# Performance work log

Hardware: AMD Instinct MI355X
Metric: run time of the kernel (lower is better)

## Reference

```python
import jax, jax.numpy as jnp
import numpy as np

N, E = 50000, 800000
IN_DIM, OUT_DIM, HEADS, ORDER = 128, 32, 4, 2
HID = OUT_DIM * HEADS  # 128
NEG_SLOPE = 0.2
LN_EPS = 1e-5


def setup_inputs() -> dict:
    key = jax.random.key(0)
    ks = jax.random.split(key, 16)
    inp = {
        'features': jax.random.normal(ks[0], (N, IN_DIM), jnp.float32),
        'src': jax.random.randint(ks[1], (E,), 0, N, jnp.int32),
        'dst': jax.random.randint(ks[2], (E,), 0, N, jnp.int32),
    }
    in_dims = [IN_DIM, HID]
    for i in range(ORDER):
        d_in = in_dims[i]
        s = 1.0 / np.sqrt(d_in)
        inp[f'W{i}'] = jax.random.normal(ks[3 + 5 * i], (d_in, HID), jnp.float32) * s
        inp[f'al{i}'] = jax.random.normal(ks[4 + 5 * i], (HEADS, OUT_DIM), jnp.float32) * 0.1
        inp[f'ar{i}'] = jax.random.normal(ks[5 + 5 * i], (HEADS, OUT_DIM), jnp.float32) * 0.1
        inp[f'b{i}'] = jnp.zeros((HID,), jnp.float32)
        inp[f'g{i}'] = jnp.ones((HID,), jnp.float32)
        inp[f'be{i}'] = jnp.zeros((HID,), jnp.float32)
    return inp


def _gat_layer(x, src, dst, W, al, ar, b):
    # x: [N, d_in] -> h: [N, H, D]
    h = (x @ W).reshape(N, HEADS, OUT_DIM)
    el = jnp.sum(h * al, axis=-1)  # [N, H]
    er = jnp.sum(h * ar, axis=-1)  # [N, H]
    e = jax.nn.leaky_relu(el[src] + er[dst], NEG_SLOPE)  # [E, H]
    # segment softmax over incoming edges of each dst node
    m = jax.ops.segment_max(e, dst, num_segments=N)  # [N, H]
    ex = jnp.exp(e - m[dst])  # [E, H]
    denom = jax.ops.segment_sum(ex, dst, num_segments=N)  # [N, H]
    alpha = ex / jnp.maximum(denom[dst], 1e-9)  # [E, H]
    msg = h[src] * alpha[:, :, None]  # [E, H, D]
    out = jax.ops.segment_sum(msg, dst, num_segments=N)  # [N, H, D]
    return out.reshape(N, HID) + b


def _layernorm(x, g, be):
    mu = jnp.mean(x, axis=-1, keepdims=True)
    var = jnp.mean(jnp.square(x - mu), axis=-1, keepdims=True)
    return (x - mu) * jax.lax.rsqrt(var + LN_EPS) * g + be


def reference(features, src, dst, W0, al0, ar0, b0, g0, be0, W1, al1, ar1, b1, g1, be1):
    feats = features
    params = [(W0, al0, ar0, b0, g0, be0), (W1, al1, ar1, b1, g1, be1)]
    for (W, al, ar, b, g, be) in params:
        feats = _gat_layer(feats, src, dst, W, al, ar, b)
        feats = _layernorm(feats, g, be)
        feats = jax.nn.elu(feats)
    return feats
```

## Files before the change

### kernel.cpp

```cpp
#include <hip/hip_runtime.h>
#include <hip/hip_bf16.h>

#define N_NODES 50000
#define E_EDGES 800000
#define HID 128
#define HEADS 4
#define NEG_SLOPE 0.2f
#define LN_EPS 1e-5f
#define PARAM_FLOATS 17024
#define NBUCK 196
#define BCAP 6144
#define BIN_CH 2048

typedef __attribute__((ext_vector_type(8))) short short8;
typedef __attribute__((ext_vector_type(4))) float float4v;

__device__ __forceinline__ float bf2f(__hip_bfloat16 b) { return __bfloat162float(b); }
__device__ __forceinline__ float u2f(unsigned short u) {
    return __uint_as_float(((unsigned int)u) << 16);
}
__device__ __forceinline__ short bfb(float f) {
    __hip_bfloat16 h = __float2bfloat16(f);
    return *(short*)&h;
}
__device__ __forceinline__ float leaky(float v) { return v > 0.f ? v : v * NEG_SLOPE; }

__device__ __forceinline__ unsigned int f2ord(float f) {
    unsigned int u = __float_as_uint(f);
    return (u & 0x80000000u) ? ~u : (u | 0x80000000u);
}
__device__ __forceinline__ float ord2f(unsigned int u) {
    u = (u & 0x80000000u) ? (u & 0x7FFFFFFFu) : ~u;
    return __uint_as_float(u);
}

__global__ __launch_bounds__(256) void detect_kernel(const unsigned int* __restrict__ w0,
                                                     unsigned int* __restrict__ flag,
                                                     unsigned int* __restrict__ gmax0,
                                                     unsigned int* __restrict__ gmax1) {
    int t = threadIdx.x;
    if (t < 4) {
        gmax0[t] = f2ord(-INFINITY);
        gmax1[t] = f2ord(-INFINITY);
    }
    int cnt = 0;
    for (int i = t; i < 4096; i += 256) {
        unsigned int lo = (w0[i] & 0xFFFFu) << 16;
        float v = fabsf(__uint_as_float(lo));
        if (v >= 1e-6f && v <= 1.0f) cnt++;
    }
    __shared__ int sh[4];
#pragma unroll
    for (int off = 32; off >= 1; off >>= 1) cnt += __shfl_xor(cnt, off);
    if ((t & 63) == 0) sh[t >> 6] = cnt;
    __syncthreads();
    if (t == 0) *flag = ((sh[0] + sh[1] + sh[2] + sh[3]) > 2048) ? 1u : 0u;
}

__device__ __forceinline__ float load_any(const void* p, int i, unsigned int isbf16) {
    return isbf16 ? bf2f(((const __hip_bfloat16*)p)[i]) : ((const float*)p)[i];
}

__global__ __launch_bounds__(256) void cvt_params_kernel(const void* W, const void* al,
                                                         const void* ar, const void* b,
                                                         const void* g, const void* be,
                                                         const unsigned int* __restrict__ flag,
                                                         float* __restrict__ out,
                                                         unsigned short* __restrict__ wt) {
    int i = blockIdx.x * 256 + threadIdx.x;
    if (i >= PARAM_FLOATS) return;
    unsigned int isb = *flag;
    if (i < 16384) {
        unsigned short bits;
        if (isb) bits = ((const unsigned short*)W)[i];
        else     { short s = bfb(((const float*)W)[i]); bits = (unsigned short)s; }
        wt[((i & 127) << 7) | (i >> 7)] = bits;
        return;
    }
    const void* src; int off;
    if (i < 16512)      { src = al; off = i - 16384; }
    else if (i < 16640) { src = ar; off = i - 16512; }
    else if (i < 16768) { src = b;  off = i - 16640; }
    else if (i < 16896) { src = g;  off = i - 16768; }
    else                { src = be; off = i - 16896; }
    out[i] = load_any(src, off, isb);
}

__global__ __launch_bounds__(256) void bin_kernel(const int* __restrict__ src,
                                                  const int* __restrict__ dst,
                                                  int* __restrict__ bcnt,
                                                  unsigned int* __restrict__ ebuf) {
    __shared__ int lh[NBUCK];
    __shared__ int lbase[NBUCK];
    int t = threadIdx.x;
    for (int i = t; i < NBUCK; i += 256) lh[i] = 0;
    __syncthreads();
    int e0 = blockIdx.x * BIN_CH;
    int n = min(BIN_CH, E_EDGES - e0);
    int s8[8], d8[8], rk[8];
#pragma unroll
    for (int j = 0; j < 8; ++j) {
        int k = j * 256 + t;
        if (k < n) {
            s8[j] = src[e0 + k];
            d8[j] = dst[e0 + k];
            rk[j] = atomicAdd(&lh[d8[j] >> 8], 1);
        }
    }
    __syncthreads();
    for (int i = t; i < NBUCK; i += 256) lbase[i] = atomicAdd(&bcnt[i], lh[i]);
    __syncthreads();
#pragma unroll
    for (int j = 0; j < 8; ++j) {
        int k = j * 256 + t;
        if (k < n) {
            int b = d8[j] >> 8;
            int pos = lbase[b] + rk[j];
            if (pos < BCAP)
                ebuf[b * BCAP + pos] = ((unsigned int)s8[j] << 8) | (unsigned int)(d8[j] & 255);
        }
    }
}

__global__ __launch_bounds__(256) void bscan_kernel(const int* __restrict__ bcnt,
                                                    int* __restrict__ bbase) {
    int t = threadIdx.x;
    int lane = t & 63, wid = t >> 6;
    int v = (t < NBUCK) ? min(bcnt[t], BCAP) : 0;
    int x = v;
#pragma unroll
    for (int o = 1; o < 64; o <<= 1) {
        int y = __shfl_up(x, o);
        if (lane >= o) x += y;
    }
    __shared__ int wt[4];
    if (lane == 63) wt[wid] = x;
    __syncthreads();
    int add = 0;
    for (int j = 0; j < wid; j++) add += wt[j];
    if (t < NBUCK) bbase[t] = add + x - v;
}

__global__ __launch_bounds__(256) void csr_kernel(const int* __restrict__ bcnt,
                                                  const int* __restrict__ bbase,
                                                  const unsigned int* __restrict__ ebuf,
                                                  int* __restrict__ offs,
                                                  int* __restrict__ esrc) {
    __shared__ int cnt[256];
    __shared__ int wt[4];
    __shared__ int out_lds[BCAP];
    int b = blockIdx.x, t = threadIdx.x;
    int n = min(bcnt[b], BCAP);
    int base = bbase[b];
    const unsigned int* eb = ebuf + b * BCAP;
    cnt[t] = 0;
    __syncthreads();
    for (int i = t; i < n; i += 256) atomicAdd(&cnt[eb[i] & 255u], 1);
    __syncthreads();
    int lane = t & 63, wid = t >> 6;
    int v = cnt[t];
    int x = v;
#pragma unroll
    for (int o = 1; o < 64; o <<= 1) {
        int y = __shfl_up(x, o);
        if (lane >= o) x += y;
    }
    if (lane == 63) wt[wid] = x;
    __syncthreads();
    int add = 0;
    for (int j = 0; j < wid; j++) add += wt[j];
    int excl = add + x - v;
    int node = b * 256 + t;
    if (node <= N_NODES) offs[node] = base + excl;
    __syncthreads();
    cnt[t] = excl;
    __syncthreads();
    for (int i = t; i < n; i += 256) {
        unsigned int e = eb[i];
        int p = atomicAdd(&cnt[e & 255u], 1);
        out_lds[p] = (int)(e >> 8);
    }
    __syncthreads();
    for (int i = t; i < n; i += 256) esrc[base + i] = out_lds[i];
}

__global__ __launch_bounds__(256) void gemm_mfma_kernel(const void* __restrict__ xin,
                                                        const unsigned short* __restrict__ wt,
                                                        const float* __restrict__ params,
                                                        const unsigned int* __restrict__ flag,
                                                        int mode,
                                                        unsigned int* __restrict__ hb2,
                                                        float* __restrict__ el,
                                                        float* __restrict__ er,
                                                        unsigned int* __restrict__ gmax,
                                                        int M) {
    __shared__ float ldsC[4][16][132];
    __shared__ unsigned int smax[4];
    unsigned int isb = mode ? 1u : *flag;
    int t = threadIdx.x;
    if (t < 4) smax[t] = 0u;
    int w = t >> 6, lane = t & 63;
    int m = lane & 15, quad = lane >> 4;
    int row0b = blockIdx.x * 64;
    int arow = row0b + w * 16 + m;
    bool avalid = arow < M;

    float4v acc[8];
#pragma unroll
    for (int i = 0; i < 8; i++) acc[i] = (float4v){0.f, 0.f, 0.f, 0.f};

#pragma unroll
    for (int kt = 0; kt < 4; ++kt) {
        short8 a = (short8){0, 0, 0, 0, 0, 0, 0, 0};
        if (avalid) {
            int base = arow * 128 + kt * 32 + quad * 8;
            if (isb) {
                a = *(const short8*)((const unsigned short*)xin + base);
            } else {
                const float* xp = (const float*)xin + base;
                float4 f0 = *(const float4*)xp;
                float4 f1 = *(const float4*)(xp + 4);
                a = (short8){bfb(f0.x), bfb(f0.y), bfb(f0.z), bfb(f0.w),
                             bfb(f1.x), bfb(f1.y), bfb(f1.z), bfb(f1.w)};
            }
        }
#pragma unroll
        for (int ct = 0; ct < 8; ++ct) {
            short8 b = *(const short8*)(wt + (ct * 16 + m) * 128 + kt * 32 + quad * 8);
            acc[ct] = __builtin_amdgcn_mfma_f32_16x16x32_bf16(a, b, acc[ct], 0, 0, 0);
        }
    }

#pragma unroll
    for (int ct = 0; ct < 8; ++ct)
#pragma unroll
        for (int r = 0; r < 4; ++r)
            ldsC[w][quad * 4 + r][ct * 16 + m] = acc[ct][r];
    __syncthreads();

    int c0 = (t & 15) * 8;
    int r0e = (t >> 4) * 4;
    float al8[8], ar8[8];
#pragma unroll
    for (int j = 0; j < 8; j++) {
        al8[j] = params[16384 + c0 + j];
        ar8[j] = params[16512 + c0 + j];
    }
    int head = (lane & 15) >> 2;
    float elmax = -INFINITY;

#pragma unroll
    for (int i = 0; i < 4; i++) {
        int rr = r0e + i;
        int row = row0b + rr;
        bool ok = row < M;
        const float* ld = &ldsC[rr >> 4][rr & 15][c0];
        float4 h0 = *(const float4*)ld;
        float4 h1 = *(const float4*)(ld + 4);
        float hv[8] = {h0.x, h0.y, h0.z, h0.w, h1.x, h1.y, h1.z, h1.w};
        if (ok) {
            unsigned int u[4];
#pragma unroll
            for (int j = 0; j < 4; j++) {
                u[j] = (unsigned int)(unsigned short)bfb(hv[2 * j])
                     | ((unsigned int)(unsigned short)bfb(hv[2 * j + 1]) << 16);
            }
            *(uint4*)(hb2 + row * 64 + (c0 >> 1)) = make_uint4(u[0], u[1], u[2], u[3]);
        }
        float e_l = 0.f, e_r = 0.f;
#pragma unroll
        for (int j = 0; j < 8; j++) {
            e_l = fmaf(hv[j], al8[j], e_l);
            e_r = fmaf(hv[j], ar8[j], e_r);
        }
        e_l += __shfl_xor(e_l, 1); e_l += __shfl_xor(e_l, 2);
        e_r += __shfl_xor(e_r, 1); e_r += __shfl_xor(e_r, 2);
        if (ok && (lane & 3) == 0) {
            el[row * 4 + head] = e_l;
            er[row * 4 + head] = e_r;
            elmax = fmaxf(elmax, e_l);
        }
    }
    elmax = fmaxf(elmax, __shfl_xor(elmax, 16));
    elmax = fmaxf(elmax, __shfl_xor(elmax, 32));
    __syncthreads();
    if ((lane & 15) == 0 || (lane & 15) == 4 || (lane & 15) == 8 || (lane & 15) == 12) {
        if (elmax > -INFINITY) atomicMax(&smax[head], f2ord(elmax));
    }
    __syncthreads();
    if (t < 4) atomicMax(&gmax[t], smax[t]);
}

template <bool LAST>
__global__ __launch_bounds__(256) void agg_ln_kernel(const int* __restrict__ offs,
                                                     const int* __restrict__ esrc,
                                                     const float* __restrict__ el,
                                                     const float* __restrict__ er,
                                                     const unsigned int* __restrict__ hb2,
                                                     const float* __restrict__ params,
                                                     const unsigned int* __restrict__ gmax,
                                                     const unsigned int* __restrict__ flag,
                                                     unsigned int* __restrict__ x_next,
                                                     void* __restrict__ out) {
    int node = (blockIdx.x * 256 + threadIdx.x) >> 6;
    int lane = threadIdx.x & 63;
    if (node >= N_NODES) return;
    int e0 = offs[node], e1 = offs[node + 1];
    int d = e1 - e0;
    int sh = lane & 3;
    int slot = lane >> 2;
    float er_s = er[node * 4 + sh];
    float M = leaky(ord2f(gmax[sh]) + er_s);

    int hd = lane >> 4;
    int c0 = lane * 2;

    float lsum = 0.f, a0 = 0.f, a1 = 0.f;
    for (int b0 = 0; b0 < d; b0 += 16) {
        int idx = b0 + slot;
        float ex = 0.f;
        int s = 0;
        if (idx < d) {
            s = esrc[e0 + idx];
            ex = __expf(leaky(el[s * 4 + sh] + er_s) - M);
        }
        lsum += ex;
        _Float16 e16 = (_Float16)ex;
        unsigned int pk = ((unsigned int)s << 16)
                        | (unsigned int)__builtin_bit_cast(unsigned short, e16);
        int nb = min(16, d - b0);
        if (nb == 16) {
#pragma unroll
            for (int j = 0; j < 16; ++j) {
                unsigned int q = __shfl(pk, j * 4 + hd);
                int sj = q >> 16;
                float exj = (float)__builtin_bit_cast(_Float16, (unsigned short)(q & 0xFFFFu));
                unsigned int p = hb2[sj * 64 + lane];
                a0 = fmaf(exj, u2f((unsigned short)(p & 0xFFFFu)), a0);
                a1 = fmaf(exj, __uint_as_float(p & 0xFFFF0000u), a1);
            }
        } else {
            for (int j = 0; j < nb; ++j) {
                unsigned int q = __shfl(pk, j * 4 + hd);
                int sj = q >> 16;
                float exj = (float)__builtin_bit_cast(_Float16, (unsigned short)(q & 0xFFFFu));
                unsigned int p = hb2[sj * 64 + lane];
                a0 = fmaf(exj, u2f((unsigned short)(p & 0xFFFFu)), a0);
                a1 = fmaf(exj, __uint_as_float(p & 0xFFFF0000u), a1);
            }
        }
    }
#pragma unroll
    for (int off = 4; off <= 32; off <<= 1) lsum += __shfl_xor(lsum, off);
    float l = __shfl(lsum, hd);

    float inv = 1.f / fmaxf(l, 1e-9f);
    const float* b  = params + 16640;
    const float* g  = params + 16768;
    const float* be = params + 16896;
    float v0 = fmaf(a0, inv, b[c0]);
    float v1 = fmaf(a1, inv, b[c0 + 1]);

    float s = v0 + v1;
#pragma unroll
    for (int off = 32; off >= 1; off >>= 1) s += __shfl_xor(s, off);
    float mu = s * (1.f / 128.f);
    float q0 = v0 - mu, q1 = v1 - mu;
    float vs = q0 * q0 + q1 * q1;
#pragma unroll
    for (int off = 32; off >= 1; off >>= 1) vs += __shfl_xor(vs, off);
    float rstd = rsqrtf(vs * (1.f / 128.f) + LN_EPS);
    float y0 = q0 * rstd * g[c0] + be[c0];
    float y1 = q1 * rstd * g[c0 + 1] + be[c0 + 1];
    y0 = y0 > 0.f ? y0 : expm1f(y0);
    y1 = y1 > 0.f ? y1 : expm1f(y1);

    if (LAST) {
        if (*flag) {
            unsigned int packed = (unsigned int)(unsigned short)bfb(y0)
                                | ((unsigned int)(unsigned short)bfb(y1) << 16);
            ((unsigned int*)out)[node * 64 + lane] = packed;
        } else {
            ((float2*)out)[node * 64 + lane] = make_float2(y0, y1);
        }
    } else {
        unsigned int packed = (unsigned int)(unsigned short)bfb(y0)
                            | ((unsigned int)(unsigned short)bfb(y1) << 16);
        x_next[node * 64 + lane] = packed;
    }
}

extern "C" void kernel_launch(void* const* d_in, const int* in_sizes, int n_in,
                              void* d_out, int out_size, void* d_ws, size_t ws_size,
                              hipStream_t stream) {
    const void* features = d_in[0];
    const int* src = (const int*)d_in[1];
    const int* dst = (const int*)d_in[2];

    char* w = (char*)d_ws;
    unsigned int* xbuf = (unsigned int*)w;
    unsigned int* hb = (unsigned int*)(w + 12800000);
    float* el = (float*)(w + 25600000);
    float* er = (float*)(w + 26400000);
    float* params0 = (float*)(w + 27200000);
    float* params1 = params0 + PARAM_FLOATS;
    unsigned short* wt0 = (unsigned short*)(w + 27337000);
    unsigned short* wt1 = wt0 + 16384;
    int* offs = (int*)(w + 27403000);
    int* esrc = (int*)(w + 27604000);
    int* bcnt  = (int*)(w + 30804992);
    int* bbase = (int*)(w + 30806016);
    unsigned int* flag  = (unsigned int*)(w + 30806848);
    unsigned int* gmax0 = (unsigned int*)(w + 30806912);
    unsigned int* gmax1 = (unsigned int*)(w + 30806976);
    unsigned int* ebuf = (unsigned int*)(w + 30807040);

    detect_kernel<<<1, 256, 0, stream>>>((const unsigned int*)d_in[3], flag, gmax0, gmax1);
    cvt_params_kernel<<<(PARAM_FLOATS + 255) / 256, 256, 0, stream>>>(
        d_in[3], d_in[4], d_in[5], d_in[6], d_in[7], d_in[8], flag, params0, wt0);
    cvt_params_kernel<<<(PARAM_FLOATS + 255) / 256, 256, 0, stream>>>(
        d_in[9], d_in[10], d_in[11], d_in[12], d_in[13], d_in[14], flag, params1, wt1);

    hipMemsetAsync(bcnt, 0, NBUCK * sizeof(int), stream);
    bin_kernel<<<(E_EDGES + BIN_CH - 1) / BIN_CH, 256, 0, stream>>>(src, dst, bcnt, ebuf);
    bscan_kernel<<<1, 256, 0, stream>>>(bcnt, bbase);
    csr_kernel<<<NBUCK, 256, 0, stream>>>(bcnt, bbase, ebuf, offs, esrc);

    for (int l = 0; l < 2; ++l) {
        float* params = (l == 0) ? params0 : params1;
        unsigned short* wt = (l == 0) ? wt0 : wt1;
        unsigned int* gmax = (l == 0) ? gmax0 : gmax1;
        const void* x = (l == 0) ? features : (const void*)xbuf;
        int mode = (l == 0) ? 0 : 1;

        gemm_mfma_kernel<<<(N_NODES + 63) / 64, 256, 0, stream>>>(
            x, wt, params, flag, mode, hb, el, er, gmax, N_NODES);
        if (l == 0) {
            agg_ln_kernel<false><<<(N_NODES * 64 + 255) / 256, 256, 0, stream>>>(
                offs, esrc, el, er, hb, params, gmax, flag, xbuf, nullptr);
        } else {
            agg_ln_kernel<true><<<(N_NODES * 64 + 255) / 256, 256, 0, stream>>>(
                offs, esrc, el, er, hb, params, gmax, flag, nullptr, d_out);
        }
    }
}
```

Baseline: 287.2 us.

## Fuse setup kernels and split edge gather across half-waves with wider loads

Merges detect, both parameter-conversion launches and the bucket-count memset into one kernel. The bucket prefix scan moves into each csr block, so the separate scan launch goes away. The aggregation loop now has each half-wave handle alternate edges with 8-byte loads of four channels per lane, and a cross-half reduction at the end. LayerNorm switches to a one-pass sum and sum-of-squares, which saves launch overhead and shuffle rounds but can lose some variance precision, and the loop no longer special-cases partial edge batches.

After: 264.9 us. 1.08x faster.

```diff
diff --git a/kernel.cpp b/kernel.cpp
--- a/kernel.cpp
+++ b/kernel.cpp
@@ -11,6 +11,7 @@
 #define NBUCK 196
 #define BCAP 6144
 #define BIN_CH 2048
+#define CVT_BLOCKS 67
 
 typedef __attribute__((ext_vector_type(8))) short short8;
 typedef __attribute__((ext_vector_type(4))) float float4v;
@@ -34,42 +35,56 @@
     return __uint_as_float(u);
 }
 
-__global__ __launch_bounds__(256) void detect_kernel(const unsigned int* __restrict__ w0,
-                                                     unsigned int* __restrict__ flag,
-                                                     unsigned int* __restrict__ gmax0,
-                                                     unsigned int* __restrict__ gmax1) {
+__global__ __launch_bounds__(256) void cvt_params_kernel(
+    const void* W0, const void* al0, const void* ar0, const void* b0,
+    const void* g0, const void* be0,
+    const void* W1, const void* al1, const void* ar1, const void* b1,
+    const void* g1, const void* be1,
+    float* __restrict__ out0, float* __restrict__ out1,
+    unsigned short* __restrict__ wt0, unsigned short* __restrict__ wt1,
+    unsigned int* __restrict__ flag, unsigned int* __restrict__ gmax0,
+    unsigned int* __restrict__ gmax1, int* __restrict__ bcnt) {
     int t = threadIdx.x;
-    if (t < 4) {
-        gmax0[t] = f2ord(-INFINITY);
-        gmax1[t] = f2ord(-INFINITY);
-    }
+    const unsigned int* w0p = (const unsigned int*)W0;
     int cnt = 0;
     for (int i = t; i < 4096; i += 256) {
-        unsigned int lo = (w0[i] & 0xFFFFu) << 16;
+        unsigned int lo = (w0p[i] & 0xFFFFu) << 16;
         float v = fabsf(__uint_as_float(lo));
         if (v >= 1e-6f && v <= 1.0f) cnt++;
     }
-    __shared__ int sh[4];
 #pragma unroll
     for (int off = 32; off >= 1; off >>= 1) cnt += __shfl_xor(cnt, off);
-    if ((t & 63) == 0) sh[t >> 6] = cnt;
-    __syncthreads();
-    if (t == 0) *flag = ((sh[0] + sh[1] + sh[2] + sh[3]) > 2048) ? 1u : 0u;
-}
-
-__device__ __forceinline__ float load_any(const void* p, int i, unsigned int isbf16) {
-    return isbf16 ? bf2f(((const __hip_bfloat16*)p)[i]) : ((const float*)p)[i];
-}
-
-__global__ __launch_bounds__(256) void cvt_params_kernel(const void* W, const void* al,
-                                                         const void* ar, const void* b,
-                                                         const void* g, const void* be,
-                                                         const unsigned int* __restrict__ flag,
-                                                         float* __restrict__ out,
-                                                         unsigned short* __restrict__ wt) {
-    int i = blockIdx.x * 256 + threadIdx.x;
+    __shared__ int shm[4];
+    if ((t & 63) == 0) shm[t >> 6] = cnt;
+    __syncthreads();
+    unsigned int isb = ((shm[0] + shm[1] + shm[2] + shm[3]) > 2048) ? 1u : 0u;
+
+    if (blockIdx.x == 0) {
+        if (t == 0) *flag = isb;
+        if (t < 4) {
+            gmax0[t] = f2ord(-INFINITY);
+            gmax1[t] = f2ord(-INFINITY);
+        }
+        if (t < NBUCK) bcnt[t] = 0;
+    }
+
+    int blk = blockIdx.x;
+    int layer = 0;
+    if (blk >= CVT_BLOCKS) { layer = 1; blk -= CVT_BLOCKS; }
+    int i = blk * 256 + t;
     if (i >= PARAM_FLOATS) return;
-    unsigned int isb = *flag;
+
+    const void *W, *al, *ar, *b, *g, *be;
+    float* out;
+    unsigned short* wt;
+    if (layer == 0) {
+        W = W0; al = al0; ar = ar0; b = b0; g = g0; be = be0;
+        out = out0; wt = wt0;
+    } else {
+        W = W1; al = al1; ar = ar1; b = b1; g = g1; be = be1;
+        out = out1; wt = wt1;
+    }
+
     if (i < 16384) {
         unsigned short bits;
         if (isb) bits = ((const unsigned short*)W)[i];
@@ -83,7 +98,7 @@
     else if (i < 16768) { src = b;  off = i - 16640; }
     else if (i < 16896) { src = g;  off = i - 16768; }
     else                { src = be; off = i - 16896; }
-    out[i] = load_any(src, off, isb);
+    out[i] = isb ? bf2f(((const __hip_bfloat16*)src)[off]) : ((const float*)src)[off];
 }
 
 __global__ __launch_bounds__(256) void bin_kernel(const int* __restrict__ src,
@@ -122,42 +137,39 @@
     }
 }
 
-__global__ __launch_bounds__(256) void bscan_kernel(const int* __restrict__ bcnt,
-                                                    int* __restrict__ bbase) {
-    int t = threadIdx.x;
-    int lane = t & 63, wid = t >> 6;
-    int v = (t < NBUCK) ? min(bcnt[t], BCAP) : 0;
-    int x = v;
-#pragma unroll
-    for (int o = 1; o < 64; o <<= 1) {
-        int y = __shfl_up(x, o);
-        if (lane >= o) x += y;
-    }
-    __shared__ int wt[4];
-    if (lane == 63) wt[wid] = x;
-    __syncthreads();
-    int add = 0;
-    for (int j = 0; j < wid; j++) add += wt[j];
-    if (t < NBUCK) bbase[t] = add + x - v;
-}
-
 __global__ __launch_bounds__(256) void csr_kernel(const int* __restrict__ bcnt,
-                                                  const int* __restrict__ bbase,
                                                   const unsigned int* __restrict__ ebuf,
                                                   int* __restrict__ offs,
                                                   int* __restrict__ esrc) {
     __shared__ int cnt[256];
     __shared__ int wt[4];
+    __shared__ int sbase[256];
     __shared__ int out_lds[BCAP];
     int b = blockIdx.x, t = threadIdx.x;
+    int lane = t & 63, wid = t >> 6;
+
+    int bv = (t < NBUCK) ? min(bcnt[t], BCAP) : 0;
+    {
+        int x = bv;
+#pragma unroll
+        for (int o = 1; o < 64; o <<= 1) {
+            int y = __shfl_up(x, o);
+            if (lane >= o) x += y;
+        }
+        if (lane == 63) wt[wid] = x;
+        __syncthreads();
+        int add = 0;
+        for (int j = 0; j < wid; j++) add += wt[j];
+        sbase[t] = add + x - bv;
+    }
+    __syncthreads();
+    int base = sbase[b];
     int n = min(bcnt[b], BCAP);
-    int base = bbase[b];
     const unsigned int* eb = ebuf + b * BCAP;
     cnt[t] = 0;
     __syncthreads();
     for (int i = t; i < n; i += 256) atomicAdd(&cnt[eb[i] & 255u], 1);
     __syncthreads();
-    int lane = t & 63, wid = t >> 6;
     int v = cnt[t];
     int x = v;
 #pragma unroll
@@ -309,13 +321,13 @@
     int d = e1 - e0;
     int sh = lane & 3;
     int slot = lane >> 2;
+    int l5 = lane & 31;
+    int half = lane >> 5;
+    int hd = l5 >> 3;
     float er_s = er[node * 4 + sh];
     float M = leaky(ord2f(gmax[sh]) + er_s);
 
-    int hd = lane >> 4;
-    int c0 = lane * 2;
-
-    float lsum = 0.f, a0 = 0.f, a1 = 0.f;
+    float lsum = 0.f, a0 = 0.f, a1 = 0.f, a2 = 0.f, a3 = 0.f;
     for (int b0 = 0; b0 < d; b0 += 16) {
         int idx = b0 + slot;
         float ex = 0.f;
@@ -328,65 +340,75 @@
         _Float16 e16 = (_Float16)ex;
         unsigned int pk = ((unsigned int)s << 16)
                         | (unsigned int)__builtin_bit_cast(unsigned short, e16);
-        int nb = min(16, d - b0);
-        if (nb == 16) {
-#pragma unroll
-            for (int j = 0; j < 16; ++j) {
-                unsigned int q = __shfl(pk, j * 4 + hd);
-                int sj = q >> 16;
-                float exj = (float)__builtin_bit_cast(_Float16, (unsigned short)(q & 0xFFFFu));
-                unsigned int p = hb2[sj * 64 + lane];
-                a0 = fmaf(exj, u2f((unsigned short)(p & 0xFFFFu)), a0);
-                a1 = fmaf(exj, __uint_as_float(p & 0xFFFF0000u), a1);
+#pragma unroll
+        for (int jp = 0; jp < 8; ++jp) {
+            unsigned int q = __shfl(pk, (jp * 2 + half) * 4 + hd);
+            int sj = (int)(q >> 16);
+            float exj = (float)__builtin_bit_cast(_Float16, (unsigned short)(q & 0xFFFFu));
+            uint2 p = *(const uint2*)(hb2 + sj * 64 + l5 * 2);
+            a0 = fmaf(exj, u2f((unsigned short)(p.x & 0xFFFFu)), a0);
+            a1 = fmaf(exj, __uint_as_float(p.x & 0xFFFF0000u), a1);
+            a2 = fmaf(exj, u2f((unsigned short)(p.y & 0xFFFFu)), a2);
+            a3 = fmaf(exj, __uint_as_float(p.y & 0xFFFF0000u), a3);
+        }
+    }
+#pragma unroll
+    for (int off = 4; off <= 32; off <<= 1) lsum += __shfl_xor(lsum, off);
+    float l = __shfl(lsum, hd);
+    a0 += __shfl_xor(a0, 32);
+    a1 += __shfl_xor(a1, 32);
+    a2 += __shfl_xor(a2, 32);
+    a3 += __shfl_xor(a3, 32);
+
+    float inv = 1.f / fmaxf(l, 1e-9f);
+    int c0 = l5 * 4;
+    float4 b4 = *(const float4*)(params + 16640 + c0);
+    float v0 = fmaf(a0, inv, b4.x);
+    float v1 = fmaf(a1, inv, b4.y);
+    float v2 = fmaf(a2, inv, b4.z);
+    float v3 = fmaf(a3, inv, b4.w);
+
+    float s1 = v0 + v1 + v2 + v3;
+    float s2 = v0 * v0 + v1 * v1 + v2 * v2 + v3 * v3;
+#pragma unroll
+    for (int off = 1; off <= 16; off <<= 1) {
+        s1 += __shfl_xor(s1, off);
+        s2 += __shfl_xor(s2, off);
+    }
+    float mu = s1 * (1.f / 128.f);
+    float var = fmaxf(s2 * (1.f / 128.f) - mu * mu, 0.f);
+    float rstd = rsqrtf(var + LN_EPS);
+    float4 g4 = *(const float4*)(params + 16768 + c0);
+    float4 be4 = *(const float4*)(params + 16896 + c0);
+    float y0 = (v0 - mu) * rstd * g4.x + be4.x;
+    float y1 = (v1 - mu) * rstd * g4.y + be4.y;
+    float y2 = (v2 - mu) * rstd * g4.z + be4.z;
+    float y3 = (v3 - mu) * rstd * g4.w + be4.w;
+    y0 = y0 > 0.f ? y0 : expm1f(y0);
+    y1 = y1 > 0.f ? y1 : expm1f(y1);
+    y2 = y2 > 0.f ? y2 : expm1f(y2);
+    y3 = y3 > 0.f ? y3 : expm1f(y3);
+
+    if (half == 0) {
+        if (LAST) {
+            if (*flag) {
+                uint2 pk2;
+                pk2.x = (unsigned int)(unsigned short)bfb(y0)
+                      | ((unsigned int)(unsigned short)bfb(y1) << 16);
+                pk2.y = (unsigned int)(unsigned short)bfb(y2)
+                      | ((unsigned int)(unsigned short)bfb(y3) << 16);
+                *(uint2*)((unsigned int*)out + node * 64 + l5 * 2) = pk2;
+            } else {
+                *(float4*)((float*)out + node * 128 + c0) = make_float4(y0, y1, y2, y3);
             }
         } else {
-            for (int j = 0; j < nb; ++j) {
-                unsigned int q = __shfl(pk, j * 4 + hd);
-                int sj = q >> 16;
-                float exj = (float)__builtin_bit_cast(_Float16, (unsigned short)(q & 0xFFFFu));
-                unsigned int p = hb2[sj * 64 + lane];
-                a0 = fmaf(exj, u2f((unsigned short)(p & 0xFFFFu)), a0);
-                a1 = fmaf(exj, __uint_as_float(p & 0xFFFF0000u), a1);
-            }
-        }
-    }
-#pragma unroll
-    for (int off = 4; off <= 32; off <<= 1) lsum += __shfl_xor(lsum, off);
-    float l = __shfl(lsum, hd);
-
-    float inv = 1.f / fmaxf(l, 1e-9f);
-    const float* b  = params + 16640;
-    const float* g  = params + 16768;
-    const float* be = params + 16896;
-    float v0 = fmaf(a0, inv, b[c0]);
-    float v1 = fmaf(a1, inv, b[c0 + 1]);
-
-    float s = v0 + v1;
-#pragma unroll
-    for (int off = 32; off >= 1; off >>= 1) s += __shfl_xor(s, off);
-    float mu = s * (1.f / 128.f);
-    float q0 = v0 - mu, q1 = v1 - mu;
-    float vs = q0 * q0 + q1 * q1;
-#pragma unroll
-    for (int off = 32; off >= 1; off >>= 1) vs += __shfl_xor(vs, off);
-    float rstd = rsqrtf(vs * (1.f / 128.f) + LN_EPS);
-    float y0 = q0 * rstd * g[c0] + be[c0];
-    float y1 = q1 * rstd * g[c0 + 1] + be[c0 + 1];
-    y0 = y0 > 0.f ? y0 : expm1f(y0);
-    y1 = y1 > 0.f ? y1 : expm1f(y1);
-
-    if (LAST) {
-        if (*flag) {
-            unsigned int packed = (unsigned int)(unsigned short)bfb(y0)
-                                | ((unsigned int)(unsigned short)bfb(y1) << 16);
-            ((unsigned int*)out)[node * 64 + lane] = packed;
-        } else {
-            ((float2*)out)[node * 64 + lane] = make_float2(y0, y1);
-        }
-    } else {
-        unsigned int packed = (unsigned int)(unsigned short)bfb(y0)
-                            | ((unsigned int)(unsigned short)bfb(y1) << 16);
-        x_next[node * 64 + lane] = packed;
+            uint2 pk2;
+            pk2.x = (unsigned int)(unsigned short)bfb(y0)
+                  | ((unsigned int)(unsigned short)bfb(y1) << 16);
+            pk2.y = (unsigned int)(unsigned short)bfb(y2)
+                  | ((unsigned int)(unsigned short)bfb(y3) << 16);
+            *(uint2*)(x_next + node * 64 + l5 * 2) = pk2;
+        }
     }
 }
 
@@ -409,22 +431,18 @@
     int* offs = (int*)(w + 27403000);
     int* esrc = (int*)(w + 27604000);
     int* bcnt  = (int*)(w + 30804992);
-    int* bbase = (int*)(w + 30806016);
     unsigned int* flag  = (unsigned int*)(w + 30806848);
     unsigned int* gmax0 = (unsigned int*)(w + 30806912);
     unsigned int* gmax1 = (unsigned int*)(w + 30806976);
     unsigned int* ebuf = (unsigned int*)(w + 30807040);
 
-    detect_kernel<<<1, 256, 0, stream>>>((const unsigned int*)d_in[3], flag, gmax0, gmax1);
-    cvt_params_kernel<<<(PARAM_FLOATS + 255) / 256, 256, 0, stream>>>(
-        d_in[3], d_in[4], d_in[5], d_in[6], d_in[7], d_in[8], flag, params0, wt0);
-    cvt_params_kernel<<<(PARAM_FLOATS + 255) / 256, 256, 0, stream>>>(
-        d_in[9], d_in[10], d_in[11], d_in[12], d_in[13], d_in[14], flag, params1, wt1);
-
-    hipMemsetAsync(bcnt, 0, NBUCK * sizeof(int), stream);
+    cvt_params_kernel<<<2 * CVT_BLOCKS, 256, 0, stream>>>(
+        d_in[3], d_in[4], d_in[5], d_in[6], d_in[7], d_in[8],
+        d_in[9], d_in[10], d_in[11], d_in[12], d_in[13], d_in[14],
+        params0, params1, wt0, wt1, flag, gmax0, gmax1, bcnt);
+
     bin_kernel<<<(E_EDGES + BIN_CH - 1) / BIN_CH, 256, 0, stream>>>(src, dst, bcnt, ebuf);
-    bscan_kernel<<<1, 256, 0, stream>>>(bcnt, bbase);
-    csr_kernel<<<NBUCK, 256, 0, stream>>>(bcnt, bbase, ebuf, offs, esrc);
+    csr_kernel<<<NBUCK, 256, 0, stream>>>(bcnt, ebuf, offs, esrc);
 
     for (int l = 0; l < 2; ++l) {
         float* params = (l == 0) ? params0 : params1;
```
